# Performance work log

Hardware: AMD Instinct MI355X
Metric: run time of the kernel (lower is better)

## Reference

```python
import jax, jax.numpy as jnp
import numpy as np

DILATION = 64
KERNEL = 2

def setup_inputs() -> dict:
    key = jax.random.key(0)
    k1, k2 = jax.random.split(key)
    x = jax.random.normal(k1, (16, 64, 16384), dtype=jnp.float32)
    w = jax.random.normal(k2, (64, 64, KERNEL), dtype=jnp.float32) * 0.1
    return {"x": x, "w": w}

def _causal_dilated_conv(x, w):
    # left-pad by dilation*(kernel_size-1) for causality
    pad = DILATION * (KERNEL - 1)
    xp = jnp.pad(x, ((0, 0), (0, 0), (pad, 0)))
    return jax.lax.conv_general_dilated(
        xp, w,
        window_strides=(1,),
        padding='VALID',
        rhs_dilation=(DILATION,),
        dimension_numbers=('NCH', 'OIH', 'NCH'))

def reference(x, w):
    y = _causal_dilated_conv(x, w)          # [B, C_out, T]
    return jnp.tanh(y) * jax.nn.sigmoid(y)  # fused gate
```

## Files before the change

### kernel.cpp

```cpp
#include <hip/hip_runtime.h>


#define B_ 16
#define C_ 64
#define T_ 16384
#define TT 128
#define HALO 64
#define RR (TT + HALO)
#define XL_OFS (RR * 64)

typedef __attribute__((ext_vector_type(8))) short short8;
typedef __attribute__((ext_vector_type(4))) float f32x4;

union Frag { short8 s; unsigned u[4]; };

__device__ __forceinline__ unsigned bf16_rne(float f) {
    unsigned u = __float_as_uint(f);
    unsigned r = 0x7fffu + ((u >> 16) & 1u);
    return (u + r) >> 16;
}

__global__ __launch_bounds__(256, 3) void conv_gate_mfma2(
    const float* __restrict__ x,
    const float* __restrict__ w,
    float* __restrict__ out)
{
    __shared__ unsigned short xs[2 * RR * 64];

    const int tid = threadIdx.x;
    const int t0  = blockIdx.x * TT;
    const int b   = blockIdx.y;
    const float* xb = x + (size_t)b * C_ * T_;

    #pragma unroll
    for (int it = 0; it < 12; ++it) {
        int task = it * 256 + tid;
        int rr   = task % RR;
        int c4   = task / RR;
        int g    = t0 - HALO + rr;
        float v0 = 0.f, v1 = 0.f, v2 = 0.f, v3 = 0.f;
        if (g >= 0) {
            const float* xp = xb + (size_t)(4 * c4) * T_ + g;
            v0 = xp[0 * T_]; v1 = xp[1 * T_]; v2 = xp[2 * T_]; v3 = xp[3 * T_];
        }
        unsigned u0 = __float_as_uint(v0), u1 = __float_as_uint(v1);
        unsigned u2 = __float_as_uint(v2), u3 = __float_as_uint(v3);
        unsigned h01 = (u0 >> 16) | (u1 & 0xffff0000u);
        unsigned h23 = (u2 >> 16) | (u3 & 0xffff0000u);
        unsigned l0 = __float_as_uint(v0 - __uint_as_float(u0 & 0xffff0000u));
        unsigned l1 = __float_as_uint(v1 - __uint_as_float(u1 & 0xffff0000u));
        unsigned l2 = __float_as_uint(v2 - __uint_as_float(u2 & 0xffff0000u));
        unsigned l3 = __float_as_uint(v3 - __uint_as_float(u3 & 0xffff0000u));
        unsigned g01 = (l0 >> 16) | (l1 & 0xffff0000u);
        unsigned g23 = (l2 >> 16) | (l3 & 0xffff0000u);
        int chunk = (c4 >> 1) ^ (rr & 7);
        int so = rr * 64 + chunk * 8 + (c4 & 1) * 4;
        *(uint2*)(&xs[so])          = make_uint2(h01, h23);
        *(uint2*)(&xs[XL_OFS + so]) = make_uint2(g01, g23);
    }

    const int lane = tid & 63;
    const int wid  = tid >> 6;
    const int m    = lane & 15;
    const int q    = lane >> 4;
    const int co   = wid * 16 + m;

    Frag wh[2][2], wl[2][2];
    #pragma unroll
    for (int h = 0; h < 2; ++h) {
        const float* wp = w + co * 128 + h * 64 + q * 16;
        float f[16];
        #pragma unroll
        for (int v = 0; v < 4; ++v) {
            float4 t4 = *(const float4*)(wp + 4 * v);
            f[4*v+0] = t4.x; f[4*v+1] = t4.y; f[4*v+2] = t4.z; f[4*v+3] = t4.w;
        }
        #pragma unroll
        for (int p = 0; p < 2; ++p) {
            #pragma unroll
            for (int d = 0; d < 4; ++d) {
                float e0 = f[2*(2*d)   + p];
                float e1 = f[2*(2*d+1) + p];
                unsigned h0 = bf16_rne(e0), h1 = bf16_rne(e1);
                float r0 = e0 - __uint_as_float(h0 << 16);
                float r1 = e1 - __uint_as_float(h1 << 16);
                wh[p][h].u[d] = h0 | (h1 << 16);
                wl[p][h].u[d] = bf16_rne(r0) | (bf16_rne(r1) << 16);
            }
        }
    }

    f32x4 acc[8];
    #pragma unroll
    for (int s = 0; s < 8; ++s) acc[s] = (f32x4){0.f, 0.f, 0.f, 0.f};

    __syncthreads();

    const int n  = m;
    const int sw = n & 7;
    #pragma unroll
    for (int u = 0; u < 12; ++u) {
        const int rbase = (16 * u + n) * 64;
        Frag fh[2], fl[2];
        #pragma unroll
        for (int h = 0; h < 2; ++h) {
            int c = (((4 * h + q) ^ sw) * 8);
            fh[h].s = *(const short8*)(&xs[rbase + c]);
            fl[h].s = *(const short8*)(&xs[XL_OFS + rbase + c]);
        }
        if (u < 8) {
            #pragma unroll
            for (int h = 0; h < 2; ++h) {
                acc[u] = __builtin_amdgcn_mfma_f32_16x16x32_bf16(wh[0][h].s, fh[h].s, acc[u], 0, 0, 0);
                acc[u] = __builtin_amdgcn_mfma_f32_16x16x32_bf16(wh[0][h].s, fl[h].s, acc[u], 0, 0, 0);
                acc[u] = __builtin_amdgcn_mfma_f32_16x16x32_bf16(wl[0][h].s, fh[h].s, acc[u], 0, 0, 0);
            }
        }
        if (u >= 4) {
            const int s2 = u - 4;
            #pragma unroll
            for (int h = 0; h < 2; ++h) {
                acc[s2] = __builtin_amdgcn_mfma_f32_16x16x32_bf16(wh[1][h].s, fh[h].s, acc[s2], 0, 0, 0);
                acc[s2] = __builtin_amdgcn_mfma_f32_16x16x32_bf16(wh[1][h].s, fl[h].s, acc[s2], 0, 0, 0);
                acc[s2] = __builtin_amdgcn_mfma_f32_16x16x32_bf16(wl[1][h].s, fh[h].s, acc[s2], 0, 0, 0);
            }
        }
    }

    float* ob = out + ((size_t)b * C_ + wid * 16) * T_ + t0;
    #pragma unroll
    for (int s = 0; s < 8; ++s) {
        #pragma unroll
        for (int r = 0; r < 4; ++r) {
            float y  = acc[s][r];
            y = fminf(fmaxf(y, -20.f), 20.f);
            float e   = __expf(-y);
            float e2  = e * e;
            float num = 1.f - e2;
            float den = (1.f + e) * (1.f + e2);
            ob[(size_t)(4 * q + r) * T_ + 16 * s + n] = num * __builtin_amdgcn_rcpf(den);
        }
    }
}

extern "C" void kernel_launch(void* const* d_in, const int* in_sizes, int n_in,
                              void* d_out, int out_size, void* d_ws, size_t ws_size,
                              hipStream_t stream) {
    const float* x = (const float*)d_in[0];
    const float* w = (const float*)d_in[1];
    float* out = (float*)d_out;
    dim3 grid(T_ / TT, B_);
    conv_gate_mfma2<<<grid, dim3(256), 0, stream>>>(x, w, out);
}
```

Before: 131.5 us.

## Drop input low-bf16 split, keep weight hi/lo split, halve LDS footprint

Inputs are now rounded to a single bf16 value (RNE) instead of a hi/lo bf16 pair, so only the weights keep the two-term split. This cuts MFMAs per step from 6 to 4 and halves the shared-memory tile. That allows launch bounds of 6 blocks per CU instead of 3, and loads 8 channels per thread with 128-bit LDS stores. Accuracy drops because activations lose the low bf16 correction term, which may matter against the fp32 reference tolerance.

```diff
diff --git a/kernel.cpp b/kernel.cpp
--- a/kernel.cpp
+++ b/kernel.cpp
@@ -7,7 +7,6 @@
 #define TT 128
 #define HALO 64
 #define RR (TT + HALO)
-#define XL_OFS (RR * 64)
 
 typedef __attribute__((ext_vector_type(8))) short short8;
 typedef __attribute__((ext_vector_type(4))) float f32x4;
@@ -16,16 +15,22 @@
 
 __device__ __forceinline__ unsigned bf16_rne(float f) {
     unsigned u = __float_as_uint(f);
-    unsigned r = 0x7fffu + ((u >> 16) & 1u);
-    return (u + r) >> 16;
+    return (u + 0x7fffu + ((u >> 16) & 1u)) >> 16;
 }
 
-__global__ __launch_bounds__(256, 3) void conv_gate_mfma2(
+__device__ __forceinline__ unsigned pack_rne(float a, float b) {
+    unsigned ua = __float_as_uint(a), ub = __float_as_uint(b);
+    unsigned ra = ua + 0x7fffu + ((ua >> 16) & 1u);
+    unsigned rb = ub + 0x7fffu + ((ub >> 16) & 1u);
+    return (ra >> 16) | (rb & 0xffff0000u);
+}
+
+__global__ __launch_bounds__(256, 6) void conv_gate_mfma3(
     const float* __restrict__ x,
     const float* __restrict__ w,
     float* __restrict__ out)
 {
-    __shared__ unsigned short xs[2 * RR * 64];
+    __shared__ unsigned short xs[RR * 64];
 
     const int tid = threadIdx.x;
     const int t0  = blockIdx.x * TT;
@@ -33,30 +38,26 @@
     const float* xb = x + (size_t)b * C_ * T_;
 
     #pragma unroll
-    for (int it = 0; it < 12; ++it) {
+    for (int it = 0; it < 6; ++it) {
         int task = it * 256 + tid;
         int rr   = task % RR;
-        int c4   = task / RR;
+        int c8   = task / RR;
         int g    = t0 - HALO + rr;
-        float v0 = 0.f, v1 = 0.f, v2 = 0.f, v3 = 0.f;
+        float v[8];
         if (g >= 0) {
-            const float* xp = xb + (size_t)(4 * c4) * T_ + g;
-            v0 = xp[0 * T_]; v1 = xp[1 * T_]; v2 = xp[2 * T_]; v3 = xp[3 * T_];
+            const float* xp = xb + (size_t)(8 * c8) * T_ + g;
+            #pragma unroll
+            for (int i = 0; i < 8; ++i) v[i] = xp[(size_t)i * T_];
+        } else {
+            #pragma unroll
+            for (int i = 0; i < 8; ++i) v[i] = 0.f;
         }
-        unsigned u0 = __float_as_uint(v0), u1 = __float_as_uint(v1);
-        unsigned u2 = __float_as_uint(v2), u3 = __float_as_uint(v3);
-        unsigned h01 = (u0 >> 16) | (u1 & 0xffff0000u);
-        unsigned h23 = (u2 >> 16) | (u3 & 0xffff0000u);
-        unsigned l0 = __float_as_uint(v0 - __uint_as_float(u0 & 0xffff0000u));
-        unsigned l1 = __float_as_uint(v1 - __uint_as_float(u1 & 0xffff0000u));
-        unsigned l2 = __float_as_uint(v2 - __uint_as_float(u2 & 0xffff0000u));
-        unsigned l3 = __float_as_uint(v3 - __uint_as_float(u3 & 0xffff0000u));
-        unsigned g01 = (l0 >> 16) | (l1 & 0xffff0000u);
-        unsigned g23 = (l2 >> 16) | (l3 & 0xffff0000u);
-        int chunk = (c4 >> 1) ^ (rr & 7);
-        int so = rr * 64 + chunk * 8 + (c4 & 1) * 4;
-        *(uint2*)(&xs[so])          = make_uint2(h01, h23);
-        *(uint2*)(&xs[XL_OFS + so]) = make_uint2(g01, g23);
+        unsigned p0 = pack_rne(v[0], v[1]);
+        unsigned p1 = pack_rne(v[2], v[3]);
+        unsigned p2 = pack_rne(v[4], v[5]);
+        unsigned p3 = pack_rne(v[6], v[7]);
+        int so = rr * 64 + ((c8 ^ (rr & 7)) * 8);
+        *(uint4*)(&xs[so]) = make_uint4(p0, p1, p2, p3);
     }
 
     const int lane = tid & 63;
@@ -71,9 +72,9 @@
         const float* wp = w + co * 128 + h * 64 + q * 16;
         float f[16];
         #pragma unroll
-        for (int v = 0; v < 4; ++v) {
-            float4 t4 = *(const float4*)(wp + 4 * v);
-            f[4*v+0] = t4.x; f[4*v+1] = t4.y; f[4*v+2] = t4.z; f[4*v+3] = t4.w;
+        for (int v4 = 0; v4 < 4; ++v4) {
+            float4 t4 = *(const float4*)(wp + 4 * v4);
+            f[4*v4+0] = t4.x; f[4*v4+1] = t4.y; f[4*v4+2] = t4.z; f[4*v4+3] = t4.w;
         }
         #pragma unroll
         for (int p = 0; p < 2; ++p) {
@@ -101,29 +102,21 @@
     #pragma unroll
     for (int u = 0; u < 12; ++u) {
         const int rbase = (16 * u + n) * 64;
-        Frag fh[2], fl[2];
-        #pragma unroll
-        for (int h = 0; h < 2; ++h) {
-            int c = (((4 * h + q) ^ sw) * 8);
-            fh[h].s = *(const short8*)(&xs[rbase + c]);
-            fl[h].s = *(const short8*)(&xs[XL_OFS + rbase + c]);
-        }
+        Frag f0, f1;
+        f0.s = *(const short8*)(&xs[rbase + ((q ^ sw) * 8)]);
+        f1.s = *(const short8*)(&xs[rbase + (((4 + q) ^ sw) * 8)]);
         if (u < 8) {
-            #pragma unroll
-            for (int h = 0; h < 2; ++h) {
-                acc[u] = __builtin_amdgcn_mfma_f32_16x16x32_bf16(wh[0][h].s, fh[h].s, acc[u], 0, 0, 0);
-                acc[u] = __builtin_amdgcn_mfma_f32_16x16x32_bf16(wh[0][h].s, fl[h].s, acc[u], 0, 0, 0);
-                acc[u] = __builtin_amdgcn_mfma_f32_16x16x32_bf16(wl[0][h].s, fh[h].s, acc[u], 0, 0, 0);
-            }
+            acc[u] = __builtin_amdgcn_mfma_f32_16x16x32_bf16(wh[0][0].s, f0.s, acc[u], 0, 0, 0);
+            acc[u] = __builtin_amdgcn_mfma_f32_16x16x32_bf16(wl[0][0].s, f0.s, acc[u], 0, 0, 0);
+            acc[u] = __builtin_amdgcn_mfma_f32_16x16x32_bf16(wh[0][1].s, f1.s, acc[u], 0, 0, 0);
+            acc[u] = __builtin_amdgcn_mfma_f32_16x16x32_bf16(wl[0][1].s, f1.s, acc[u], 0, 0, 0);
         }
         if (u >= 4) {
             const int s2 = u - 4;
-            #pragma unroll
-            for (int h = 0; h < 2; ++h) {
-                acc[s2] = __builtin_amdgcn_mfma_f32_16x16x32_bf16(wh[1][h].s, fh[h].s, acc[s2], 0, 0, 0);
-                acc[s2] = __builtin_amdgcn_mfma_f32_16x16x32_bf16(wh[1][h].s, fl[h].s, acc[s2], 0, 0, 0);
-                acc[s2] = __builtin_amdgcn_mfma_f32_16x16x32_bf16(wl[1][h].s, fh[h].s, acc[s2], 0, 0, 0);
-            }
+            acc[s2] = __builtin_amdgcn_mfma_f32_16x16x32_bf16(wh[1][0].s, f0.s, acc[s2], 0, 0, 0);
+            acc[s2] = __builtin_amdgcn_mfma_f32_16x16x32_bf16(wl[1][0].s, f0.s, acc[s2], 0, 0, 0);
+            acc[s2] = __builtin_amdgcn_mfma_f32_16x16x32_bf16(wh[1][1].s, f1.s, acc[s2], 0, 0, 0);
+            acc[s2] = __builtin_amdgcn_mfma_f32_16x16x32_bf16(wl[1][1].s, f1.s, acc[s2], 0, 0, 0);
         }
     }
 
@@ -150,5 +143,5 @@
     const float* w = (const float*)d_in[1];
     float* out = (float*)d_out;
     dim3 grid(T_ / TT, B_);
-    conv_gate_mfma2<<<grid, dim3(256), 0, stream>>>(x, w, out);
+    conv_gate_mfma3<<<grid, dim3(256), 0, stream>>>(x, w, out);
 }
```

After: 123.4 us. -6.2%, faster.
